# Kernel tuning notes

Hardware: AMD Instinct MI355X
Metric: run time of the kernel (lower is better)

The kernel has to match this reference:

```python
import jax, jax.numpy as jnp
from jax import lax
import numpy as np

M = 40000   # query points
N = 40000   # support points (== M -> non-strided layer)
H = 16      # neighbors per query
C = 128     # in_channels == out_channels
K = 15      # kernel points (shell_sizes=[1,14])
G = 8       # attention groups
CPG = C // G  # channels per group = 16
RADIUS = 2.5
SIGMA = 2.0
INF = 1.0e6
NEG_SLOPE = 0.1  # LeakyReLU(0.1)


def _make_kernel_points():
    # deterministic stand-in for load_kernels(): center point + points in sphere of given radius
    rng = np.random.RandomState(42)
    kp = rng.randn(K, 3).astype(np.float32)
    kp[0] = 0.0  # fixed 'center' kernel point
    nrm = np.linalg.norm(kp[1:], axis=1, keepdims=True)
    kp[1:] = kp[1:] / nrm * (rng.uniform(0.3, 1.0, (K - 1, 1)).astype(np.float32) * RADIUS)
    return jnp.asarray(kp)


def setup_inputs() -> dict:
    key = jax.random.key(0)
    ks = jax.random.split(key, 10)
    s_pts = jax.random.uniform(ks[0], (N, 3), jnp.float32) * 2.0  # points in a 2m box
    q_pts = s_pts  # same-resolution layer: M == N
    s_feats = jax.random.normal(ks[1], (N, C), jnp.float32)
    neighb_inds = jax.random.randint(ks[2], (M, H), 0, N)
    sc = 1.0 / np.sqrt(C)
    return {
        "q_pts": q_pts,
        "s_pts": s_pts,
        "s_feats": s_feats,
        "neighb_inds": neighb_inds,
        "kernel_points": _make_kernel_points(),          # (K, 3) buffer
        "weights": jax.random.normal(ks[3], (K, C), jnp.float32) * sc,  # per-kernel-point weights
        "Wq": jax.random.normal(ks[4], (C, C), jnp.float32) * sc,
        "bq": jnp.zeros((C,), jnp.float32),
        "Wk": jax.random.normal(ks[5], (C, C), jnp.float32) * sc,
        "bk": jnp.zeros((C,), jnp.float32),
        "alpha_w1": jax.random.normal(ks[6], (C, CPG), jnp.float32) * sc,   # alpha_mlp Linear(C->CpG), no bias
        "alpha_w2": jax.random.normal(ks[7], (CPG, CPG), jnp.float32) * (1.0 / np.sqrt(CPG)),  # final Linear, bias
        "alpha_b2": jnp.zeros((CPG,), jnp.float32),
    }


def _leaky(x):
    return jnp.where(x >= 0, x, NEG_SLOPE * x)


def reference(q_pts, s_pts, s_feats, neighb_inds, kernel_points, weights,
              Wq, bq, Wk, bk, alpha_w1, alpha_w2, alpha_b2):
    # ---- kernel-point influences (torch.no_grad in original) ----
    qp = lax.stop_gradient(q_pts)
    sp = lax.stop_gradient(s_pts)
    kp = lax.stop_gradient(kernel_points)
    sp_pad = jnp.concatenate([sp, jnp.full((1, 3), INF, sp.dtype)], axis=0)  # shadow point
    neighbors = sp_pad[neighb_inds] - qp[:, None, :]                          # (M, H, 3)
    diff = neighbors[:, :, None, :] - kp[None, None, :, :]                    # (M, H, K, 3)
    sq_d = jnp.sum(diff * diff, axis=-1)                                      # (M, H, K)
    nn_sq = jnp.min(sq_d, axis=-1)                                            # (M, H)
    nn_idx = jnp.argmin(sq_d, axis=-1)                                        # (M, H)
    infl = jnp.clip(1.0 - jnp.sqrt(nn_sq) / SIGMA, 0.0)                       # 'linear' influence

    # ---- value branch (linear_v is Identity since C_in == C_out) ----
    v_pad = jnp.concatenate([s_feats, jnp.zeros((1, C), s_feats.dtype)], axis=0)
    neighb_v = v_pad[neighb_inds]                                             # (M, H, C)

    # ---- KPConv merge: gather per-kernel-point weights, scale by influence, multiply ----
    nw = weights[nn_idx] * infl[..., None]                                    # (M, H, C)
    neighb_v = neighb_v * nw

    # ---- grouped attention branch ----
    k_feats = s_feats @ Wk + bk
    k_pad = jnp.concatenate([k_feats, jnp.zeros((1, C), k_feats.dtype)], axis=0)
    neighb_k = k_pad[neighb_inds]                                             # (M, H, C)
    q_feats = s_feats @ Wq + bq                                               # (M, C) since M == N

    a = q_feats[:, None, :] - neighb_k                                        # (M, H, C)
    # alpha_mlp with norm_type='none': ['NA', CpG, 'NA', CpG] -> act, linear, act, linear(+bias)
    a = _leaky(a)
    a = a @ alpha_w1                                                          # (M, H, CpG)
    a = _leaky(a)
    a = a @ alpha_w2 + alpha_b2                                               # (M, H, CpG)
    a = jax.nn.sigmoid(a)                                                     # attention_act='sigmoid'

    # apply group-shared attention weights and aggregate over neighbors (sum)
    nv = neighb_v.reshape(M, H, G, CPG) * a[:, :, None, :]                    # (M, H, G, CpG)
    out = jnp.sum(nv, axis=1).reshape(M, C)                                   # (M, C_out)
    return out
```

## Files before the change

kernel.cpp:

```cpp
#include <hip/hip_runtime.h>
#include <math.h>

#define Mq 40000
#define Cc 128
#define Hh 16
#define Kk 15

typedef unsigned int uint32;
typedef unsigned short ushortT;
typedef short bf16x8 __attribute__((ext_vector_type(8)));
typedef float f32x4 __attribute__((ext_vector_type(4)));

static __device__ __forceinline__ uint32 f2bf_rne(float f) {
    union { float f; uint32 u; } v; v.f = f;
    return (v.u + 0x7FFFu + ((v.u >> 16) & 1u)) >> 16;
}
static __device__ __forceinline__ float bflo(uint32 u) { return __uint_as_float(u << 16); }
static __device__ __forceinline__ float bfhi(uint32 u) { return __uint_as_float(u & 0xFFFF0000u); }
static __device__ __forceinline__ uint32 cvtpk(float a, float b) {
    uint32 r; asm("v_cvt_pk_bf16_f32 %0, %1, %2" : "=v"(r) : "v"(a), "v"(b)); return r;
}

__global__ __launch_bounds__(256) void prep(
    const float* __restrict__ s_feats, const float* __restrict__ Wq,
    const float* __restrict__ Wk,
    ushortT* __restrict__ s_bf16, ushortT* __restrict__ wT)
{
    const int b = blockIdx.x, t = threadIdx.x;
    if (b < 2500) {
        const int i = b * 256 + t;
        const float4 a = ((const float4*)s_feats)[i * 2];
        const float4 c = ((const float4*)s_feats)[i * 2 + 1];
        uint4 o;
        o.x = cvtpk(a.x, a.y); o.y = cvtpk(a.z, a.w);
        o.z = cvtpk(c.x, c.y); o.w = cvtpk(c.z, c.w);
        ((uint4*)s_bf16)[i] = o;
    } else {
        const int j = (b - 2500) * 256 + t;
        const int k = j >> 5;
        const int n0 = (j & 31) * 8;
        const float* __restrict__ src = (n0 < 128) ? (Wq + k * 128 + n0)
                                                   : (Wk + k * 128 + n0 - 128);
        #pragma unroll
        for (int e = 0; e < 8; ++e)
            wT[(n0 + e) * 128 + k] = (ushortT)f2bf_rne(src[e]);
    }
}

__global__ __launch_bounds__(256) void qk_gemm(
    const ushortT* __restrict__ s_bf16, const ushortT* __restrict__ wT,
    const float* __restrict__ bq, const float* __restrict__ bk,
    ushortT* __restrict__ q_bf16, ushortT* __restrict__ k_bf16)
{
    const int tid = threadIdx.x;
    const int w = tid >> 6, l = tid & 63;
    const int lo = l & 15, hi = l >> 4;
    const int rowblk = blockIdx.x >> 2, nblk = blockIdx.x & 3;
    const int r0 = rowblk * 64 + w * 16;
    const int n0 = nblk * 64;

    f32x4 acc[4];
    #pragma unroll
    for (int ns = 0; ns < 4; ++ns) {
        const int n = n0 + ns * 16 + lo;
        const float bv = (n < 128) ? bq[n] : bk[n - 128];
        acc[ns] = (f32x4){bv, bv, bv, bv};
    }
    #pragma unroll
    for (int kt = 0; kt < 4; ++kt) {
        const bf16x8 af = *(const bf16x8*)(s_bf16 + (r0 + lo) * Cc + kt * 32 + hi * 8);
        #pragma unroll
        for (int ns = 0; ns < 4; ++ns) {
            const int n = n0 + ns * 16 + lo;
            const bf16x8 bf = *(const bf16x8*)(wT + n * Cc + kt * 32 + hi * 8);
            acc[ns] = __builtin_amdgcn_mfma_f32_16x16x32_bf16(af, bf, acc[ns], 0, 0, 0);
        }
    }
    ushortT* __restrict__ tbl = (n0 < 128) ? q_bf16 : k_bf16;
    const int nbase = n0 & 127;
    #pragma unroll
    for (int ns = 0; ns < 4; ++ns) {
        const int col = nbase + ns * 16 + lo;
        #pragma unroll
        for (int r = 0; r < 4; ++r) {
            const int row = r0 + hi * 4 + r;
            tbl[row * Cc + col] = (ushortT)f2bf_rne(acc[ns][r]);
        }
    }
}

__global__ __launch_bounds__(256) void kpt_main(
    const float* __restrict__ q_pts, const float* __restrict__ s_pts,
    const ushortT* __restrict__ s_bf16, const int* __restrict__ nb,
    const float* __restrict__ kpts, const float* __restrict__ wkp,
    const float* __restrict__ w1, const float* __restrict__ w2,
    const float* __restrict__ b2,
    const ushortT* __restrict__ q_bf16, const ushortT* __restrict__ k_bf16,
    float* __restrict__ out)
{
    __shared__ __align__(16) uint32 wt_lds[Kk][64];
    __shared__ __align__(16) float  kpl[45];
    __shared__ __align__(16) uint32 a_u[4][1024];
    __shared__ __align__(16) float  t_scr[4][16][36];
    __shared__ __align__(16) float  sg_scr[4][16][18];
    __shared__ __align__(16) int    id_l[4][4][16];
    __shared__ __align__(16) float  in_l[4][4][16];

    const int tid = threadIdx.x;
    const int w = tid >> 6, l = tid & 63;
    const int lo = l & 15, hi = l >> 4;

    for (int i = tid; i < Kk * 64; i += 256) {
        const int k = i >> 6, c2 = i & 63;
        const float2 v = *(const float2*)(wkp + k * Cc + c2 * 2);
        wt_lds[k][c2] = cvtpk(v.x, v.y);
    }
    if (tid < 45) kpl[tid] = kpts[tid];
    #pragma unroll
    for (int r = 0; r < 4; ++r) t_scr[w][lo][16 + hi * 4 + r] = 0.f;
    __syncthreads();

    const int mq0 = blockIdx.x * 16 + w * 4;

    {
        const int m = mq0 + hi, h = lo;
        const int id = nb[m * Hh + h];
        const float px = s_pts[id * 3 + 0] - q_pts[m * 3 + 0];
        const float py = s_pts[id * 3 + 1] - q_pts[m * 3 + 1];
        const float pz = s_pts[id * 3 + 2] - q_pts[m * 3 + 2];
        float best = 1e30f; int bi = 0;
        #pragma unroll
        for (int k = 0; k < Kk; ++k) {
            const float dx = px - kpl[k * 3 + 0];
            const float dy = py - kpl[k * 3 + 1];
            const float dz = pz - kpl[k * 3 + 2];
            const float d = dx * dx + dy * dy + dz * dz;
            if (d < best) { best = d; bi = k; }
        }
        id_l[w][hi][h] = id | (bi << 20);
        in_l[w][hi][h] = fmaxf(0.f, 1.f - sqrtf(best) * 0.5f);
    }

    bf16x8 w1f[4];
    #pragma unroll
    for (int kt = 0; kt < 4; ++kt) {
        float tmp[8];
        #pragma unroll
        for (int e = 0; e < 8; ++e)
            tmp[e] = w1[(kt * 32 + hi * 8 + e) * 16 + lo];
        uint32 u[4] = {cvtpk(tmp[0], tmp[1]), cvtpk(tmp[2], tmp[3]),
                       cvtpk(tmp[4], tmp[5]), cvtpk(tmp[6], tmp[7])};
        w1f[kt] = *(bf16x8*)u;
    }
    bf16x8 w2f;
    {
        float tmp[8];
        #pragma unroll
        for (int e = 0; e < 8; ++e) {
            const int k = hi * 8 + e;
            tmp[e] = (k < 16) ? w2[k * 16 + lo] : 0.f;
        }
        uint32 u[4] = {cvtpk(tmp[0], tmp[1]), cvtpk(tmp[2], tmp[3]),
                       cvtpk(tmp[4], tmp[5]), cvtpk(tmp[6], tmp[7])};
        w2f = *(bf16x8*)u;
    }
    const float bias2 = b2[lo];
    __syncthreads();

    for (int qq = 0; qq < 4; ++qq) {
        const int m = mq0 + qq;
        int ids[16];
        #pragma unroll
        for (int h = 0; h < Hh; ++h) ids[h] = id_l[w][qq][h];

        const uint32 qv = *(const uint32*)(q_bf16 + m * Cc + 2 * l);
        const float q0 = bflo(qv), q1 = bfhi(qv);

        uint32 kv[16], vv[16];
        #pragma unroll
        for (int h = 0; h < Hh; ++h) {
            const int id = ids[h] & 0xFFFFF;
            kv[h] = *(const uint32*)(k_bf16 + id * Cc + 2 * l);
            vv[h] = *(const uint32*)(s_bf16 + id * Cc + 2 * l);
        }
        #pragma unroll
        for (int h = 0; h < Hh; ++h) {
            float a0 = q0 - bflo(kv[h]); a0 = fmaxf(a0, 0.1f * a0);
            float a1 = q1 - bfhi(kv[h]); a1 = fmaxf(a1, 0.1f * a1);
            a_u[w][(h * 64 + l) ^ ((h & 7) << 2)] = cvtpk(a0, a1);
        }
        __syncthreads();

        f32x4 acc1 = {0.f, 0.f, 0.f, 0.f};
        #pragma unroll
        for (int kt = 0; kt < 4; ++kt) {
            const int boff = (lo * 256 + kt * 64 + hi * 16) ^ ((l & 7) << 4);
            const bf16x8 af = *(const bf16x8*)((const char*)&a_u[w][0] + boff);
            acc1 = __builtin_amdgcn_mfma_f32_16x16x32_bf16(af, w1f[kt], acc1, 0, 0, 0);
        }
        #pragma unroll
        for (int r = 0; r < 4; ++r) {
            const float v = acc1[r];
            t_scr[w][hi * 4 + r][lo] = fmaxf(v, 0.1f * v);
        }
        __syncthreads();

        f32x4 acc2 = {bias2, bias2, bias2, bias2};
        {
            const float4 ta = *(const float4*)&t_scr[w][lo][hi * 8];
            const float4 tb = *(const float4*)&t_scr[w][lo][hi * 8 + 4];
            uint32 u[4] = {cvtpk(ta.x, ta.y), cvtpk(ta.z, ta.w),
                           cvtpk(tb.x, tb.y), cvtpk(tb.z, tb.w)};
            const bf16x8 tf = *(const bf16x8*)u;
            acc2 = __builtin_amdgcn_mfma_f32_16x16x32_bf16(tf, w2f, acc2, 0, 0, 0);
        }
        #pragma unroll
        for (int r = 0; r < 4; ++r) {
            const float s = 1.f / (1.f + __expf(-acc2[r]));
            sg_scr[w][hi * 4 + r][lo] = s * in_l[w][qq][hi * 4 + r];
        }
        __syncthreads();

        float o0 = 0.f, o1 = 0.f;
        #pragma unroll
        for (int h = 0; h < Hh; ++h) {
            const uint32 wp = wt_lds[ids[h] >> 20][l];
            const float2 sp = *(const float2*)&sg_scr[w][h][2 * (l & 7)];
            o0 = fmaf(bflo(vv[h]) * bflo(wp), sp.x, o0);
            o1 = fmaf(bfhi(vv[h]) * bfhi(wp), sp.y, o1);
        }
        *(float2*)(out + m * Cc + 2 * l) = make_float2(o0, o1);
    }
}

extern "C" void kernel_launch(void* const* d_in, const int* in_sizes, int n_in,
                              void* d_out, int out_size, void* d_ws, size_t ws_size,
                              hipStream_t stream) {
    const float* q_pts   = (const float*)d_in[0];
    const float* s_pts   = (const float*)d_in[1];
    const float* s_feats = (const float*)d_in[2];
    const int*   nb      = (const int*)d_in[3];
    const float* kpts    = (const float*)d_in[4];
    const float* wkp     = (const float*)d_in[5];
    const float* Wq      = (const float*)d_in[6];
    const float* bq      = (const float*)d_in[7];
    const float* Wk      = (const float*)d_in[8];
    const float* bk      = (const float*)d_in[9];
    const float* w1      = (const float*)d_in[10];
    const float* w2      = (const float*)d_in[11];
    const float* b2      = (const float*)d_in[12];
    float* outp = (float*)d_out;

    ushortT* s_bf16 = (ushortT*)d_ws;
    ushortT* q_bf16 = s_bf16 + (size_t)Mq * Cc;
    ushortT* k_bf16 = q_bf16 + (size_t)Mq * Cc;
    ushortT* wT     = k_bf16 + (size_t)Mq * Cc;

    prep    <<<2516, 256, 0, stream>>>(s_feats, Wq, Wk, s_bf16, wT);
    qk_gemm <<<2500, 256, 0, stream>>>(s_bf16, wT, bq, bk, q_bf16, k_bf16);
    kpt_main<<<2500, 256, 0, stream>>>(q_pts, s_pts, s_bf16, nb, kpts, wkp,
                                       w1, w2, b2, q_bf16, k_bf16, outp);
}
```

Measured before the change: 175.0 us.

## Fuse feature bf16 conversion into QK GEMM and use wave-local fences

The s_feats fp32-to-bf16 conversion moves into the QK GEMM, so each block loads its 64 rows once, writes the bf16 copy, and computes all 256 Q/K output columns. This removes the separate conversion pass and the re-read of s_bf16, and the GEMM grid shrinks from 2500 to 625 blocks. In the main kernel, block-wide __syncthreads are replaced by a wave-local lgkmcnt wait plus sched_barrier, since each wave touches only its own LDS slices. The t_scr padding is shrunk and zero-filled lanes replace the zeroed padding, and launch bounds now request 4 blocks per CU.

```diff
diff --git a/kernel.cpp b/kernel.cpp
--- a/kernel.cpp
+++ b/kernel.cpp
@@ -20,76 +20,66 @@
 static __device__ __forceinline__ uint32 cvtpk(float a, float b) {
     uint32 r; asm("v_cvt_pk_bf16_f32 %0, %1, %2" : "=v"(r) : "v"(a), "v"(b)); return r;
 }
-
-__global__ __launch_bounds__(256) void prep(
-    const float* __restrict__ s_feats, const float* __restrict__ Wq,
-    const float* __restrict__ Wk,
-    ushortT* __restrict__ s_bf16, ushortT* __restrict__ wT)
+#define WAVE_FENCE() do { \
+    asm volatile("s_waitcnt lgkmcnt(0)" ::: "memory"); \
+    __builtin_amdgcn_sched_barrier(0); } while (0)
+
+__global__ __launch_bounds__(256) void prepW(
+    const float* __restrict__ Wq, const float* __restrict__ Wk,
+    ushortT* __restrict__ wT)
 {
-    const int b = blockIdx.x, t = threadIdx.x;
-    if (b < 2500) {
-        const int i = b * 256 + t;
-        const float4 a = ((const float4*)s_feats)[i * 2];
-        const float4 c = ((const float4*)s_feats)[i * 2 + 1];
-        uint4 o;
-        o.x = cvtpk(a.x, a.y); o.y = cvtpk(a.z, a.w);
-        o.z = cvtpk(c.x, c.y); o.w = cvtpk(c.z, c.w);
-        ((uint4*)s_bf16)[i] = o;
-    } else {
-        const int j = (b - 2500) * 256 + t;
-        const int k = j >> 5;
-        const int n0 = (j & 31) * 8;
-        const float* __restrict__ src = (n0 < 128) ? (Wq + k * 128 + n0)
-                                                   : (Wk + k * 128 + n0 - 128);
-        #pragma unroll
-        for (int e = 0; e < 8; ++e)
-            wT[(n0 + e) * 128 + k] = (ushortT)f2bf_rne(src[e]);
-    }
-}
-
-__global__ __launch_bounds__(256) void qk_gemm(
-    const ushortT* __restrict__ s_bf16, const ushortT* __restrict__ wT,
+    const int j = blockIdx.x * 256 + threadIdx.x;
+    const int k = j >> 5;
+    const int n0 = (j & 31) * 8;
+    const float* __restrict__ src = (n0 < 128) ? (Wq + k * 128 + n0)
+                                               : (Wk + k * 128 + n0 - 128);
+    #pragma unroll
+    for (int e = 0; e < 8; ++e)
+        wT[(n0 + e) * 128 + k] = (ushortT)f2bf_rne(src[e]);
+}
+
+__global__ __launch_bounds__(256, 4) void qk_gemm(
+    const float* __restrict__ s_feats, const ushortT* __restrict__ wT,
     const float* __restrict__ bq, const float* __restrict__ bk,
-    ushortT* __restrict__ q_bf16, ushortT* __restrict__ k_bf16)
+    ushortT* __restrict__ s_bf16, ushortT* __restrict__ q_bf16,
+    ushortT* __restrict__ k_bf16)
 {
     const int tid = threadIdx.x;
     const int w = tid >> 6, l = tid & 63;
     const int lo = l & 15, hi = l >> 4;
-    const int rowblk = blockIdx.x >> 2, nblk = blockIdx.x & 3;
-    const int r0 = rowblk * 64 + w * 16;
-    const int n0 = nblk * 64;
-
-    f32x4 acc[4];
-    #pragma unroll
-    for (int ns = 0; ns < 4; ++ns) {
-        const int n = n0 + ns * 16 + lo;
+    const int r0 = blockIdx.x * 64 + w * 16;
+
+    bf16x8 af[4];
+    #pragma unroll
+    for (int kt = 0; kt < 4; ++kt) {
+        const float* __restrict__ p = s_feats + (size_t)(r0 + lo) * Cc + kt * 32 + hi * 8;
+        const float4 x = *(const float4*)p;
+        const float4 y = *(const float4*)(p + 4);
+        uint32 u[4] = {cvtpk(x.x, x.y), cvtpk(x.z, x.w),
+                       cvtpk(y.x, y.y), cvtpk(y.z, y.w)};
+        af[kt] = *(bf16x8*)u;
+        *(uint4*)(s_bf16 + (size_t)(r0 + lo) * Cc + kt * 32 + hi * 8) = *(uint4*)u;
+    }
+
+    #pragma unroll
+    for (int ns = 0; ns < 16; ++ns) {
+        const int n = ns * 16 + lo;
         const float bv = (n < 128) ? bq[n] : bk[n - 128];
-        acc[ns] = (f32x4){bv, bv, bv, bv};
-    }
-    #pragma unroll
-    for (int kt = 0; kt < 4; ++kt) {
-        const bf16x8 af = *(const bf16x8*)(s_bf16 + (r0 + lo) * Cc + kt * 32 + hi * 8);
-        #pragma unroll
-        for (int ns = 0; ns < 4; ++ns) {
-            const int n = n0 + ns * 16 + lo;
+        f32x4 acc = (f32x4){bv, bv, bv, bv};
+        #pragma unroll
+        for (int kt = 0; kt < 4; ++kt) {
             const bf16x8 bf = *(const bf16x8*)(wT + n * Cc + kt * 32 + hi * 8);
-            acc[ns] = __builtin_amdgcn_mfma_f32_16x16x32_bf16(af, bf, acc[ns], 0, 0, 0);
-        }
-    }
-    ushortT* __restrict__ tbl = (n0 < 128) ? q_bf16 : k_bf16;
-    const int nbase = n0 & 127;
-    #pragma unroll
-    for (int ns = 0; ns < 4; ++ns) {
-        const int col = nbase + ns * 16 + lo;
-        #pragma unroll
-        for (int r = 0; r < 4; ++r) {
-            const int row = r0 + hi * 4 + r;
-            tbl[row * Cc + col] = (ushortT)f2bf_rne(acc[ns][r]);
-        }
-    }
-}
-
-__global__ __launch_bounds__(256) void kpt_main(
+            acc = __builtin_amdgcn_mfma_f32_16x16x32_bf16(af[kt], bf, acc, 0, 0, 0);
+        }
+        ushortT* __restrict__ tbl = (ns < 8) ? q_bf16 : k_bf16;
+        const int col = n & 127;
+        #pragma unroll
+        for (int r = 0; r < 4; ++r)
+            tbl[(size_t)(r0 + hi * 4 + r) * Cc + col] = (ushortT)f2bf_rne(acc[r]);
+    }
+}
+
+__global__ __launch_bounds__(256, 4) void kpt_main(
     const float* __restrict__ q_pts, const float* __restrict__ s_pts,
     const ushortT* __restrict__ s_bf16, const int* __restrict__ nb,
     const float* __restrict__ kpts, const float* __restrict__ wkp,
@@ -101,7 +91,7 @@
     __shared__ __align__(16) uint32 wt_lds[Kk][64];
     __shared__ __align__(16) float  kpl[45];
     __shared__ __align__(16) uint32 a_u[4][1024];
-    __shared__ __align__(16) float  t_scr[4][16][36];
+    __shared__ __align__(16) float  t_scr[4][16][20];
     __shared__ __align__(16) float  sg_scr[4][16][18];
     __shared__ __align__(16) int    id_l[4][4][16];
     __shared__ __align__(16) float  in_l[4][4][16];
@@ -116,8 +106,6 @@
         wt_lds[k][c2] = cvtpk(v.x, v.y);
     }
     if (tid < 45) kpl[tid] = kpts[tid];
-    #pragma unroll
-    for (int r = 0; r < 4; ++r) t_scr[w][lo][16 + hi * 4 + r] = 0.f;
     __syncthreads();
 
     const int mq0 = blockIdx.x * 16 + w * 4;
@@ -165,7 +153,7 @@
         w2f = *(bf16x8*)u;
     }
     const float bias2 = b2[lo];
-    __syncthreads();
+    WAVE_FENCE();
 
     for (int qq = 0; qq < 4; ++qq) {
         const int m = mq0 + qq;
@@ -173,15 +161,15 @@
         #pragma unroll
         for (int h = 0; h < Hh; ++h) ids[h] = id_l[w][qq][h];
 
-        const uint32 qv = *(const uint32*)(q_bf16 + m * Cc + 2 * l);
+        const uint32 qv = *(const uint32*)(q_bf16 + (size_t)m * Cc + 2 * l);
         const float q0 = bflo(qv), q1 = bfhi(qv);
 
         uint32 kv[16], vv[16];
         #pragma unroll
         for (int h = 0; h < Hh; ++h) {
             const int id = ids[h] & 0xFFFFF;
-            kv[h] = *(const uint32*)(k_bf16 + id * Cc + 2 * l);
-            vv[h] = *(const uint32*)(s_bf16 + id * Cc + 2 * l);
+            kv[h] = *(const uint32*)(k_bf16 + (size_t)id * Cc + 2 * l);
+            vv[h] = *(const uint32*)(s_bf16 + (size_t)id * Cc + 2 * l);
         }
         #pragma unroll
         for (int h = 0; h < Hh; ++h) {
@@ -189,7 +177,7 @@
             float a1 = q1 - bfhi(kv[h]); a1 = fmaxf(a1, 0.1f * a1);
             a_u[w][(h * 64 + l) ^ ((h & 7) << 2)] = cvtpk(a0, a1);
         }
-        __syncthreads();
+        WAVE_FENCE();
 
         f32x4 acc1 = {0.f, 0.f, 0.f, 0.f};
         #pragma unroll
@@ -203,15 +191,19 @@
             const float v = acc1[r];
             t_scr[w][hi * 4 + r][lo] = fmaxf(v, 0.1f * v);
         }
-        __syncthreads();
+        WAVE_FENCE();
 
         f32x4 acc2 = {bias2, bias2, bias2, bias2};
         {
-            const float4 ta = *(const float4*)&t_scr[w][lo][hi * 8];
-            const float4 tb = *(const float4*)&t_scr[w][lo][hi * 8 + 4];
-            uint32 u[4] = {cvtpk(ta.x, ta.y), cvtpk(ta.z, ta.w),
-                           cvtpk(tb.x, tb.y), cvtpk(tb.z, tb.w)};
-            const bf16x8 tf = *(const bf16x8*)u;
+            uint32 u0 = 0, u1 = 0, u2 = 0, u3 = 0;
+            if (hi < 2) {
+                const float4 ta = *(const float4*)&t_scr[w][lo][hi * 8];
+                const float4 tb = *(const float4*)&t_scr[w][lo][hi * 8 + 4];
+                u0 = cvtpk(ta.x, ta.y); u1 = cvtpk(ta.z, ta.w);
+                u2 = cvtpk(tb.x, tb.y); u3 = cvtpk(tb.z, tb.w);
+            }
+            uint32 uu[4] = {u0, u1, u2, u3};
+            const bf16x8 tf = *(const bf16x8*)uu;
             acc2 = __builtin_amdgcn_mfma_f32_16x16x32_bf16(tf, w2f, acc2, 0, 0, 0);
         }
         #pragma unroll
@@ -219,7 +211,7 @@
             const float s = 1.f / (1.f + __expf(-acc2[r]));
             sg_scr[w][hi * 4 + r][lo] = s * in_l[w][qq][hi * 4 + r];
         }
-        __syncthreads();
+        WAVE_FENCE();
 
         float o0 = 0.f, o1 = 0.f;
         #pragma unroll
@@ -229,7 +221,7 @@
             o0 = fmaf(bflo(vv[h]) * bflo(wp), sp.x, o0);
             o1 = fmaf(bfhi(vv[h]) * bfhi(wp), sp.y, o1);
         }
-        *(float2*)(out + m * Cc + 2 * l) = make_float2(o0, o1);
+        *(float2*)(out + (size_t)m * Cc + 2 * l) = make_float2(o0, o1);
     }
 }
 
@@ -256,8 +248,8 @@
     ushortT* k_bf16 = q_bf16 + (size_t)Mq * Cc;
     ushortT* wT     = k_bf16 + (size_t)Mq * Cc;
 
-    prep    <<<2516, 256, 0, stream>>>(s_feats, Wq, Wk, s_bf16, wT);
-    qk_gemm <<<2500, 256, 0, stream>>>(s_bf16, wT, bq, bk, q_bf16, k_bf16);
+    prepW   <<<16,   256, 0, stream>>>(Wq, Wk, wT);
+    qk_gemm <<<625,  256, 0, stream>>>(s_feats, wT, bq, bk, s_bf16, q_bf16, k_bf16);
     kpt_main<<<2500, 256, 0, stream>>>(q_pts, s_pts, s_bf16, nb, kpts, wkp,
                                        w1, w2, b2, q_bf16, k_bf16, outp);
 }
```

After: 173.3 us. No clear change (-1.0%).
